# Kernel tuning notes

Measured on AMD Instinct MI355X. Metric: run time of the kernel, lower is better.

The kernel has to match this reference:

```python
import jax, jax.numpy as jnp
import numpy as np

B, C, H, W = 64, 2048, 24, 8
NUM_IDS = 751


def setup_inputs() -> dict:
    key = jax.random.key(0)
    k1, k2, k3 = jax.random.split(key, 3)
    features_map = jax.random.normal(k1, (B, C, H, W), dtype=jnp.float32)
    classifier_weight = jax.random.normal(k2, (NUM_IDS, C), dtype=jnp.float32) * 0.02
    pids = jax.random.randint(k3, (B,), 0, NUM_IDS, dtype=jnp.int64)
    return {"features_map": features_map, "classifier_weight": classifier_weight, "pids": pids}


def reference(features_map, classifier_weight, pids):
    b, c, h, w = features_map.shape
    # gather one classifier weight row per sample: [B, C]
    wrows = classifier_weight[pids]
    # per-sample 1xC @ Cx(H*W) matmul -> heatmap [B, H, W]
    heat = jnp.einsum('bc,bchw->bhw', wrows, features_map)
    hflat = heat.reshape(b, h * w)
    mn = hflat.min(axis=-1, keepdims=True)
    mx = hflat.max(axis=-1, keepdims=True)
    # original: normalize only if max != 0
    hflat = jnp.where(mx != 0, (hflat - mn) / (mx - mn), hflat)
    heat = jax.lax.stop_gradient(hflat.reshape(b, h, w))  # heatmap is detached
    return features_map * heat[:, None, :, :]
```

## Files before the change

### kernel.cpp

```cpp
#include <hip/hip_runtime.h>

#define BB 64
#define CC 2048
#define HWL 192
#define NCHUNK 16
#define CCHUNK 128

__global__ void heat_partial_kernel(const float* __restrict__ f,
                                    const float* __restrict__ w,
                                    const int* __restrict__ pids,
                                    float* __restrict__ partial) {
    const int blk = blockIdx.x;
    const int b = blk >> 4;
    const int k = blk & (NCHUNK - 1);
    const int t = threadIdx.x;

    __shared__ float ws[CCHUNK];
    const int row = pids[b];
    if (t < CCHUNK) ws[t] = w[(size_t)row * CC + k * CCHUNK + t];
    __syncthreads();

    const float* fb = f + (size_t)b * CC * HWL + (size_t)k * CCHUNK * HWL;
    float acc = 0.f;
#pragma unroll 8
    for (int c = 0; c < CCHUNK; ++c) {
        acc = fmaf(ws[c], fb[(size_t)c * HWL + t], acc);
    }
    partial[((size_t)(b * NCHUNK) + k) * HWL + t] = acc;
}

__global__ void heat_norm_kernel(const float* __restrict__ partial,
                                 float* __restrict__ heat) {
    const int b = blockIdx.x;
    const int t = threadIdx.x;
    float v = 0.f;
#pragma unroll
    for (int k = 0; k < NCHUNK; ++k)
        v += partial[((size_t)(b * NCHUNK) + k) * HWL + t];

    __shared__ float vals[HWL];
    __shared__ float s_mn, s_mx;
    vals[t] = v;
    __syncthreads();

    if (t < 64) {
        float a0 = vals[t], a1 = vals[t + 64], a2 = vals[t + 128];
        float mn = fminf(a0, fminf(a1, a2));
        float mx = fmaxf(a0, fmaxf(a1, a2));
        for (int off = 32; off > 0; off >>= 1) {
            mn = fminf(mn, __shfl_down(mn, off));
            mx = fmaxf(mx, __shfl_down(mx, off));
        }
        if (t == 0) { s_mn = mn; s_mx = mx; }
    }
    __syncthreads();

    const float mn = s_mn, mx = s_mx;
    const float out = (mx != 0.f) ? (v - mn) / (mx - mn) : v;
    heat[(size_t)b * HWL + t] = out;
}

__global__ void scale_kernel(const float4* __restrict__ f4,
                             const float4* __restrict__ heat4,
                             float4* __restrict__ out4, int n4) {
    const int i = blockIdx.x * blockDim.x + threadIdx.x;
    if (i >= n4) return;
    const int per_b4 = CC * HWL / 4;
    const int hw4n = HWL / 4;
    const int b = i / per_b4;
    const int hw4 = i % hw4n;
    const float4 h = heat4[(size_t)b * hw4n + hw4];
    const float4 v = f4[i];
    out4[i] = make_float4(v.x * h.x, v.y * h.y, v.z * h.z, v.w * h.w);
}

extern "C" void kernel_launch(void* const* d_in, const int* in_sizes, int n_in,
                              void* d_out, int out_size, void* d_ws, size_t ws_size,
                              hipStream_t stream) {
    const float* features = (const float*)d_in[0];
    const float* weight   = (const float*)d_in[1];
    const int*   pids     = (const int*)d_in[2];
    float* out = (float*)d_out;

    float* partial = (float*)d_ws;
    float* heat    = partial + (size_t)BB * NCHUNK * HWL;

    heat_partial_kernel<<<BB * NCHUNK, HWL, 0, stream>>>(features, weight, pids, partial);
    heat_norm_kernel<<<BB, HWL, 0, stream>>>(partial, heat);

    const int n4 = BB * CC * HWL / 4;
    scale_kernel<<<n4 / 256, 256, 0, stream>>>((const float4*)features,
                                               (const float4*)heat,
                                               (float4*)out, n4);
}
```

Before: 195.9 us.

## Fuse heatmap normalization into scale kernel and vectorize partial reduction loads

```diff
diff --git a/kernel.cpp b/kernel.cpp
--- a/kernel.cpp
+++ b/kernel.cpp
@@ -2,76 +2,114 @@
 
 #define BB 64
 #define CC 2048
-#define HWL 192
+#define HWN 192
+#define HW4 48
 #define NCHUNK 16
 #define CCHUNK 128
+#define CSLICE 32
+#define NSLICE (CC / CSLICE)
 
-__global__ void heat_partial_kernel(const float* __restrict__ f,
-                                    const float* __restrict__ w,
-                                    const int* __restrict__ pids,
-                                    float* __restrict__ partial) {
+__global__ void __launch_bounds__(192) heat_partial_kernel(
+    const float* __restrict__ f,
+    const float* __restrict__ w,
+    const int* __restrict__ pids,
+    float* __restrict__ partial)
+{
     const int blk = blockIdx.x;
     const int b = blk >> 4;
     const int k = blk & (NCHUNK - 1);
-    const int t = threadIdx.x;
+    const int tid = threadIdx.x;
+    const int hw4 = tid % HW4;
+    const int cl  = tid / HW4;
 
     __shared__ float ws[CCHUNK];
+    __shared__ __align__(16) float4 red[HWN];
+
     const int row = pids[b];
-    if (t < CCHUNK) ws[t] = w[(size_t)row * CC + k * CCHUNK + t];
+    if (tid < CCHUNK) ws[tid] = w[(size_t)row * CC + k * CCHUNK + tid];
     __syncthreads();
 
-    const float* fb = f + (size_t)b * CC * HWL + (size_t)k * CCHUNK * HWL;
-    float acc = 0.f;
+    const size_t base = ((size_t)b * CC + (size_t)k * CCHUNK) * HW4;
+    const float4* fb4 = (const float4*)f + base;
+
+    float4 acc = make_float4(0.f, 0.f, 0.f, 0.f);
 #pragma unroll 8
-    for (int c = 0; c < CCHUNK; ++c) {
-        acc = fmaf(ws[c], fb[(size_t)c * HWL + t], acc);
+    for (int c = cl; c < CCHUNK; c += 4) {
+        float4 v = fb4[(size_t)c * HW4 + hw4];
+        float wv = ws[c];
+        acc.x = fmaf(wv, v.x, acc.x);
+        acc.y = fmaf(wv, v.y, acc.y);
+        acc.z = fmaf(wv, v.z, acc.z);
+        acc.w = fmaf(wv, v.w, acc.w);
     }
-    partial[((size_t)(b * NCHUNK) + k) * HWL + t] = acc;
+    red[tid] = acc;
+    __syncthreads();
+    if (tid < HW4) {
+        float4 a0 = red[tid], a1 = red[tid + 48], a2 = red[tid + 96], a3 = red[tid + 144];
+        float4 s = make_float4(a0.x + a1.x + a2.x + a3.x,
+                               a0.y + a1.y + a2.y + a3.y,
+                               a0.z + a1.z + a2.z + a3.z,
+                               a0.w + a1.w + a2.w + a3.w);
+        ((float4*)partial)[(size_t)(b * NCHUNK + k) * HW4 + tid] = s;
+    }
 }
 
-__global__ void heat_norm_kernel(const float* __restrict__ partial,
-                                 float* __restrict__ heat) {
-    const int b = blockIdx.x;
-    const int t = threadIdx.x;
+__global__ void __launch_bounds__(256) norm_scale_kernel(
+    const float* __restrict__ f,
+    const float* __restrict__ partial,
+    float* __restrict__ out)
+{
+    const int blk = blockIdx.x;
+    const int b  = blk / NSLICE;
+    const int ck = blk % NSLICE;
+    const int tid = threadIdx.x;
+
+    __shared__ __align__(16) float vals[HWN];
+    __shared__ __align__(16) float hl[HWN];
+    __shared__ float s_mn, s_mx;
+
     float v = 0.f;
+    if (tid < HWN) {
+        const float* pb = partial + (size_t)b * NCHUNK * HWN + tid;
 #pragma unroll
-    for (int k = 0; k < NCHUNK; ++k)
-        v += partial[((size_t)(b * NCHUNK) + k) * HWL + t];
-
-    __shared__ float vals[HWL];
-    __shared__ float s_mn, s_mx;
-    vals[t] = v;
+        for (int kk = 0; kk < NCHUNK; ++kk)
+            v += pb[(size_t)kk * HWN];
+        vals[tid] = v;
+    }
     __syncthreads();
 
-    if (t < 64) {
-        float a0 = vals[t], a1 = vals[t + 64], a2 = vals[t + 128];
-        float mn = fminf(a0, fminf(a1, a2));
-        float mx = fmaxf(a0, fmaxf(a1, a2));
+    if (tid < 64) {
+        float m0 = vals[tid], m1 = vals[tid + 64], m2 = vals[tid + 128];
+        float mn = fminf(m0, fminf(m1, m2));
+        float mx = fmaxf(m0, fmaxf(m1, m2));
         for (int off = 32; off > 0; off >>= 1) {
             mn = fminf(mn, __shfl_down(mn, off));
             mx = fmaxf(mx, __shfl_down(mx, off));
         }
-        if (t == 0) { s_mn = mn; s_mx = mx; }
+        if (tid == 0) { s_mn = mn; s_mx = mx; }
     }
     __syncthreads();
 
-    const float mn = s_mn, mx = s_mx;
-    const float out = (mx != 0.f) ? (v - mn) / (mx - mn) : v;
-    heat[(size_t)b * HWL + t] = out;
-}
+    if (tid < HWN) {
+        const float mn = s_mn, mx = s_mx;
+        hl[tid] = (mx != 0.f) ? (v - mn) / (mx - mn) : v;
+    }
+    __syncthreads();
 
-__global__ void scale_kernel(const float4* __restrict__ f4,
-                             const float4* __restrict__ heat4,
-                             float4* __restrict__ out4, int n4) {
-    const int i = blockIdx.x * blockDim.x + threadIdx.x;
-    if (i >= n4) return;
-    const int per_b4 = CC * HWL / 4;
-    const int hw4n = HWL / 4;
-    const int b = i / per_b4;
-    const int hw4 = i % hw4n;
-    const float4 h = heat4[(size_t)b * hw4n + hw4];
-    const float4 v = f4[i];
-    out4[i] = make_float4(v.x * h.x, v.y * h.y, v.z * h.z, v.w * h.w);
+    const size_t base = ((size_t)b * CC + (size_t)ck * CSLICE) * HW4;
+    const float4* fb4 = (const float4*)f + base;
+    float4* ob4 = (float4*)out + base;
+    const float4* h4 = (const float4*)hl;
+
+#pragma unroll
+    for (int it = 0; it < (CSLICE * HW4) / 256; ++it) {
+        const int idx = it * 256 + tid;
+        const int hw4 = idx % HW4;
+        const float4 hv = h4[hw4];
+        float4 x = fb4[idx];
+        x.x *= hv.x; x.y *= hv.y; x.z *= hv.z; x.w *= hv.w;
+        ob4[idx] = x;
+    }
 }
 
 extern "C" void kernel_launch(void* const* d_in, const int* in_sizes, int n_in,
@@ -81,15 +119,8 @@
     const float* weight   = (const float*)d_in[1];
     const int*   pids     = (const int*)d_in[2];
     float* out = (float*)d_out;
+    float* partial = (float*)d_ws;
 
-    float* partial = (float*)d_ws;
-    float* heat    = partial + (size_t)BB * NCHUNK * HWL;
-
-    heat_partial_kernel<<<BB * NCHUNK, HWL, 0, stream>>>(features, weight, pids, partial);
-    heat_norm_kernel<<<BB, HWL, 0, stream>>>(partial, heat);
-
-    const int n4 = BB * CC * HWL / 4;
-    scale_kernel<<<n4 / 256, 256, 0, stream>>>((const float4*)features,
-                                               (const float4*)heat,
-                                               (float4*)out, n4);
+    heat_partial_kernel<<<BB * NCHUNK, HWN, 0, stream>>>(features, weight, pids, partial);
+    norm_scale_kernel<<<BB * NSLICE, 256, 0, stream>>>(features, partial, out);
 }
```

Measured after the change: 195.2 us. No clear change (-0.3%).
